# Kernel optimization log

Measured on AMD Instinct MI355X. Metric: run time of the kernel, lower is better.

## Reference

```python
import jax, jax.numpy as jnp
import numpy as np

NEG_SLOPE = 0.2  # PyG GATConv default leaky_relu slope
EPS = 1e-16


def gat_conv(x, W, att_src, att_dst, bias, src, dst, num_nodes, heads, out_ch, concat):
    # x: [N, F_in]; W: [F_in, heads*out_ch]
    h = (x @ W).reshape(num_nodes, heads, out_ch)          # [N, H, C]
    a_src = jnp.sum(h * att_src, axis=-1)                  # [N, H]
    a_dst = jnp.sum(h * att_dst, axis=-1)                  # [N, H]
    alpha = jax.nn.leaky_relu(a_src[src] + a_dst[dst], NEG_SLOPE)  # [E, H]
    # segment softmax over incoming edges of each destination node
    amax = jax.ops.segment_max(alpha, dst, num_segments=num_nodes)  # [N, H]
    ex = jnp.exp(alpha - amax[dst])                        # [E, H]
    denom = jax.ops.segment_sum(ex, dst, num_segments=num_nodes)    # [N, H]
    attn = ex / (denom[dst] + EPS)                         # [E, H]
    msg = h[src] * attn[:, :, None]                        # [E, H, C]
    out = jax.ops.segment_sum(msg, dst, num_segments=num_nodes)     # [N, H, C]
    if concat:
        out = out.reshape(num_nodes, heads * out_ch)
    else:
        out = out.mean(axis=1)
    return out + bias


def setup_inputs() -> dict:
    key = jax.random.key(0)
    ks = jax.random.split(key, 10)
    N, E, F_in, H, C, OUT = 50000, 800000, 512, 4, 64, 40
    x = jax.random.normal(ks[0], (N, F_in), dtype=jnp.float32)
    edge_index = jax.random.randint(ks[1], (2, E), 0, N, dtype=jnp.int64)
    s1 = (2.0 / (F_in + H * C)) ** 0.5
    s2 = (2.0 / (H * C + OUT)) ** 0.5
    return {
        "x": x,
        "edge_index": edge_index,
        "W1": jax.random.normal(ks[2], (F_in, H * C), dtype=jnp.float32) * s1,
        "att_src1": jax.random.normal(ks[3], (H, C), dtype=jnp.float32) * 0.1,
        "att_dst1": jax.random.normal(ks[4], (H, C), dtype=jnp.float32) * 0.1,
        "b1": jnp.zeros((H * C,), dtype=jnp.float32),
        "W2": jax.random.normal(ks[5], (H * C, OUT), dtype=jnp.float32) * s2,
        "att_src2": jax.random.normal(ks[6], (1, OUT), dtype=jnp.float32) * 0.1,
        "att_dst2": jax.random.normal(ks[7], (1, OUT), dtype=jnp.float32) * 0.1,
        "b2": jnp.zeros((OUT,), dtype=jnp.float32),
    }


def reference(x, edge_index, W1, att_src1, att_dst1, b1, W2, att_src2, att_dst2, b2):
    N = x.shape[0]
    H, C = att_src1.shape
    OUT = att_src2.shape[1]
    # PyG GATConv default: add self-loops
    loops = jnp.arange(N, dtype=edge_index.dtype)
    src = jnp.concatenate([edge_index[0], loops])
    dst = jnp.concatenate([edge_index[1], loops])
    # dropout is identity in eval mode
    h = gat_conv(x, W1, att_src1, att_dst1, b1, src, dst, N, H, C, concat=True)
    h = jax.nn.elu(h)
    out = gat_conv(h, W2, att_src2, att_dst2, b2, src, dst, N, 1, OUT, concat=False)
    return jax.nn.log_softmax(out, axis=1)
```

## Files before the change

### kernel.cpp

```cpp
#include <hip/hip_runtime.h>
#include <math.h>

#define FIN   512
#define H1DIM 256
#define HEADS 4
#define CH    64
#define OUTC  40
#define NEG   0.2f
#define EPSV  1e-16f
#define BK    64

__device__ __forceinline__ float leaky(float a) { return fmaxf(a, NEG * a); }

__device__ __forceinline__ short f2bf(float f) {
    unsigned u = __builtin_bit_cast(unsigned, f);
    u += 0x7FFFu + ((u >> 16) & 1u);
    return (short)(u >> 16);
}
__device__ __forceinline__ float bf2f(short s) {
    return __builtin_bit_cast(float, ((unsigned)(unsigned short)s) << 16);
}
__device__ __forceinline__ unsigned cvtpk(float lo, float hi) {
    unsigned r;
    asm("v_cvt_pk_bf16_f32 %0, %1, %2" : "=v"(r) : "v"(lo), "v"(hi));
    return r;
}
__device__ __forceinline__ float lo16(unsigned u) {
    return __builtin_bit_cast(float, u << 16);
}
__device__ __forceinline__ float hi16(unsigned u) {
    return __builtin_bit_cast(float, u & 0xffff0000u);
}

typedef __attribute__((ext_vector_type(8))) short short8;
typedef __attribute__((ext_vector_type(4))) short short4_t;
typedef __attribute__((ext_vector_type(4))) float float4_t;

typedef unsigned int u32;
typedef const __attribute__((address_space(1))) u32 gu32;
typedef __attribute__((address_space(3))) u32 lu32;

__device__ __forceinline__ void load_lds16(const void* g, void* l) {
    __builtin_amdgcn_global_load_lds((gu32*)g, (lu32*)l, 16, 0, 0);
}

__global__ void cvt_w1_kernel(const float* __restrict__ W1, short* __restrict__ w1t)
{
    int idx = blockIdx.x * 256 + threadIdx.x;
    if (idx >= FIN * H1DIM) return;
    int k = idx >> 8;
    int n = idx & 255;
    w1t[(size_t)n * FIN + k] = f2bf(W1[idx]);
}

__global__ __launch_bounds__(256) void gemm1_mfma_kernel(
    const float* __restrict__ x, const short* __restrict__ w1t,
    const float* __restrict__ attS, const float* __restrict__ attD,
    short* __restrict__ h1b, float* __restrict__ aS1, float* __restrict__ aD1, int N)
{
    __shared__ float Alf[64 * BK];
    __shared__ short Bls[256 * BK];

    const int tid  = threadIdx.x;
    const int lane = tid & 63;
    const int wid  = tid >> 6;
    const int row0 = blockIdx.x * 64;
    const int col0 = wid * 64;
    const int quad = lane >> 4;
    const int m16  = lane & 15;

    const int achunk = ((tid & 15) ^ (tid >> 4)) * 4;
    const float* asrcA[4];
#pragma unroll
    for (int p = 0; p < 4; ++p) {
        int r = row0 + p * 16 + (tid >> 4);
        if (r >= N) r = N - 1;
        asrcA[p] = x + (size_t)r * FIN + achunk;
    }

    const int trow = tid >> 3;
    const int bswz = ((tid & 7) ^ (trow & 7)) * 8;
    const short* bsrc[8];
#pragma unroll
    for (int p = 0; p < 8; ++p)
        bsrc[p] = w1t + (size_t)(p * 32 + trow) * FIN + bswz;

    float4_t acc[4][4];
#pragma unroll
    for (int i = 0; i < 4; ++i)
#pragma unroll
        for (int j = 0; j < 4; ++j) acc[i][j] = (float4_t){0.f, 0.f, 0.f, 0.f};

    const int swzB = (m16 & 7);

    for (int k0 = 0; k0 < FIN; k0 += BK) {
#pragma unroll
        for (int p = 0; p < 4; ++p)
            load_lds16(asrcA[p] + k0, Alf + p * 1024 + tid * 4);
#pragma unroll
        for (int p = 0; p < 8; ++p)
            load_lds16(bsrc[p] + k0, Bls + p * 2048 + tid * 8);
        __syncthreads();

#pragma unroll
        for (int half = 0; half < 2; ++half) {
            short8 a[4], b[4];
#pragma unroll
            for (int i = 0; i < 4; ++i) {
                int row = i * 16 + m16;
                int c0 = (quad + 4 * half) * 2;
                float4 f0 = *(const float4*)&Alf[row * BK + ((c0 ^ m16) * 4)];
                float4 f1 = *(const float4*)&Alf[row * BK + (((c0 + 1) ^ m16) * 4)];
                unsigned* tp = (unsigned*)&a[i];
                tp[0] = cvtpk(f0.x, f0.y);
                tp[1] = cvtpk(f0.z, f0.w);
                tp[2] = cvtpk(f1.x, f1.y);
                tp[3] = cvtpk(f1.z, f1.w);
            }
#pragma unroll
            for (int j = 0; j < 4; ++j) {
                int col = col0 + j * 16 + m16;
                int sub = (quad + 4 * half) ^ swzB;
                b[j] = *(const short8*)&Bls[col * BK + sub * 8];
            }
#pragma unroll
            for (int i = 0; i < 4; ++i)
#pragma unroll
                for (int j = 0; j < 4; ++j)
                    acc[i][j] = __builtin_amdgcn_mfma_f32_16x16x32_bf16(a[i], b[j], acc[i][j], 0, 0, 0);
        }
        __syncthreads();
    }

    float attSv[4], attDv[4];
#pragma unroll
    for (int j = 0; j < 4; ++j) {
        attSv[j] = attS[col0 + j * 16 + m16];
        attDv[j] = attD[col0 + j * 16 + m16];
    }

#pragma unroll
    for (int i = 0; i < 4; ++i) {
#pragma unroll
        for (int r = 0; r < 4; ++r) {
            int row = row0 + i * 16 + quad * 4 + r;
            if (row < N) {
#pragma unroll
                for (int j = 0; j < 4; ++j)
                    h1b[(size_t)row * H1DIM + col0 + j * 16 + m16] = f2bf(acc[i][j][r]);
            }
            float ps = acc[i][0][r] * attSv[0] + acc[i][1][r] * attSv[1]
                     + acc[i][2][r] * attSv[2] + acc[i][3][r] * attSv[3];
            float pd = acc[i][0][r] * attDv[0] + acc[i][1][r] * attDv[1]
                     + acc[i][2][r] * attDv[2] + acc[i][3][r] * attDv[3];
#pragma unroll
            for (int off = 1; off < 16; off <<= 1) {
                ps += __shfl_xor(ps, off);
                pd += __shfl_xor(pd, off);
            }
            if (m16 == 0 && row < N) {
                aS1[(size_t)row * 4 + wid] = ps;
                aD1[(size_t)row * 4 + wid] = pd;
            }
        }
    }
}

__global__ void degcount_kernel(const int* __restrict__ ei, int* __restrict__ deg,
                                int E, int Etot)
{
    int e = blockIdx.x * 256 + threadIdx.x;
    if (e >= Etot) return;
    int d = (e < E) ? ei[E + e] : (e - E);
    atomicAdd(&deg[d], 1);
}

__global__ __launch_bounds__(1024) void scan_partial_kernel(
    const int* __restrict__ deg, int* __restrict__ offsets,
    int* __restrict__ bsums, int N)
{
    __shared__ int wsums[16];
    __shared__ int excl[16];
    int tid = threadIdx.x, lane = tid & 63, wid = tid >> 6;
    int idx = blockIdx.x * 1024 + tid;
    int v = (idx < N) ? deg[idx] : 0;
    int sv = v;
#pragma unroll
    for (int off = 1; off < 64; off <<= 1) {
        int t = __shfl_up(sv, off, 64);
        if (lane >= off) sv += t;
    }
    if (lane == 63) wsums[wid] = sv;
    __syncthreads();
    if (wid == 0 && lane < 16) {
        int wv = wsums[lane];
        int sw = wv;
#pragma unroll
        for (int off = 1; off < 16; off <<= 1) {
            int t = __shfl_up(sw, off, 64);
            if (lane >= off) sw += t;
        }
        excl[lane] = sw - wv;
        if (lane == 15) bsums[blockIdx.x] = sw;
    }
    __syncthreads();
    if (idx < N) offsets[idx + 1] = sv + excl[wid];
}

__global__ __launch_bounds__(1024) void scan_tops_kernel(
    int* __restrict__ bsums, int* __restrict__ boffs, int nb)
{
    __shared__ int wsums[16];
    __shared__ int excl[16];
    int tid = threadIdx.x, lane = tid & 63, wid = tid >> 6;
    int v = (tid < nb) ? bsums[tid] : 0;
    int sv = v;
#pragma unroll
    for (int off = 1; off < 64; off <<= 1) {
        int t = __shfl_up(sv, off, 64);
        if (lane >= off) sv += t;
    }
    if (lane == 63) wsums[wid] = sv;
    __syncthreads();
    if (wid == 0 && lane < 16) {
        int wv = wsums[lane];
        int sw = wv;
#pragma unroll
        for (int off = 1; off < 16; off <<= 1) {
            int t = __shfl_up(sw, off, 64);
            if (lane >= off) sw += t;
        }
        excl[lane] = sw - wv;
    }
    __syncthreads();
    if (tid < nb) boffs[tid] = sv + excl[wid] - v;
}

__global__ __launch_bounds__(1024) void scan_add_kernel(
    int* __restrict__ offsets, const int* __restrict__ boffs, int N)
{
    int idx = blockIdx.x * 1024 + threadIdx.x;
    if (idx == 0) offsets[0] = 0;
    if (idx < N) offsets[idx + 1] += boffs[blockIdx.x];
}

__global__ void scatter_kernel(const int* __restrict__ ei, const int* __restrict__ offsets,
                               int* __restrict__ cursor, int* __restrict__ csr_src,
                               int E, int Etot)
{
    int e = blockIdx.x * 256 + threadIdx.x;
    if (e >= Etot) return;
    int s, d;
    if (e < E) { s = ei[e]; d = ei[E + e]; }
    else       { s = e - E; d = s; }
    int pos = offsets[d] + atomicAdd(&cursor[d], 1);
    csr_src[pos] = s;
}

__global__ __launch_bounds__(256) void agg1_kernel(
    const short* __restrict__ h1b, const float* __restrict__ aS,
    const float* __restrict__ aD, const int* __restrict__ offsets,
    const int* __restrict__ csr_src, const float* __restrict__ b1,
    short* __restrict__ g1b, int N)
{
    int lane = threadIdx.x & 63, wid = threadIdx.x >> 6;
    int half = lane >> 5;
    int l32  = lane & 31;
    int n = blockIdx.x * 4 + wid;
    if (n >= N) return;
    int start = offsets[n], end = offsets[n + 1];
    int h = l32 >> 3;
    int cbase = l32 * 8;
    float adh = aD[(size_t)n * 4 + h];

    float ac[8];
#pragma unroll
    for (int c = 0; c < 8; ++c) ac[c] = 0.f;
    float denom = 0.f;

    int p = start;
    for (; p + 4 <= end; p += 4) {
        int sA0 = csr_src[p],     sB0 = csr_src[p + 1];
        int sA1 = csr_src[p + 2], sB1 = csr_src[p + 3];
        int s0 = half ? sB0 : sA0;
        int s1 = half ? sB1 : sA1;
        float t0 = aS[(size_t)s0 * 4 + h] + adh;
        float t1 = aS[(size_t)s1 * 4 + h] + adh;
        short8 r0 = *(const short8*)&h1b[(size_t)s0 * H1DIM + cbase];
        short8 r1 = *(const short8*)&h1b[(size_t)s1 * H1DIM + cbase];
        float w0 = __expf(leaky(t0));
        float w1 = __expf(leaky(t1));
        denom += w0 + w1;
        const unsigned* u0 = (const unsigned*)&r0;
        const unsigned* u1 = (const unsigned*)&r1;
#pragma unroll
        for (int k = 0; k < 4; ++k) {
            ac[2 * k]     += w0 * lo16(u0[k]) + w1 * lo16(u1[k]);
            ac[2 * k + 1] += w0 * hi16(u0[k]) + w1 * hi16(u1[k]);
        }
    }
    for (; p + 2 <= end; p += 2) {
        int sA = csr_src[p], sB = csr_src[p + 1];
        int s = half ? sB : sA;
        float t = aS[(size_t)s * 4 + h] + adh;
        short8 r = *(const short8*)&h1b[(size_t)s * H1DIM + cbase];
        float w = __expf(leaky(t));
        denom += w;
        const unsigned* u = (const unsigned*)&r;
#pragma unroll
        for (int k = 0; k < 4; ++k) {
            ac[2 * k]     += w * lo16(u[k]);
            ac[2 * k + 1] += w * hi16(u[k]);
        }
    }
    if (p < end) {
        int s = csr_src[p];
        float t = aS[(size_t)s * 4 + h] + adh;
        short8 r = *(const short8*)&h1b[(size_t)s * H1DIM + cbase];
        float w = half ? 0.f : __expf(leaky(t));
        denom += w;
        const unsigned* u = (const unsigned*)&r;
#pragma unroll
        for (int k = 0; k < 4; ++k) {
            ac[2 * k]     += w * lo16(u[k]);
            ac[2 * k + 1] += w * hi16(u[k]);
        }
    }

    denom += __shfl_xor(denom, 32);
#pragma unroll
    for (int c = 0; c < 8; ++c) ac[c] += __shfl_xor(ac[c], 32);

    if (half == 0) {
        float inv = 1.f / (denom + EPSV);
        float4 b0 = *(const float4*)&b1[cbase];
        float4 b4 = *(const float4*)&b1[cbase + 4];
        float v[8];
        v[0] = ac[0] * inv + b0.x;
        v[1] = ac[1] * inv + b0.y;
        v[2] = ac[2] * inv + b0.z;
        v[3] = ac[3] * inv + b0.w;
        v[4] = ac[4] * inv + b4.x;
        v[5] = ac[5] * inv + b4.y;
        v[6] = ac[6] * inv + b4.z;
        v[7] = ac[7] * inv + b4.w;
#pragma unroll
        for (int c = 0; c < 8; ++c) v[c] = v[c] > 0.f ? v[c] : expm1f(v[c]);
        short8 o;
        unsigned* op = (unsigned*)&o;
        op[0] = cvtpk(v[0], v[1]);
        op[1] = cvtpk(v[2], v[3]);
        op[2] = cvtpk(v[4], v[5]);
        op[3] = cvtpk(v[6], v[7]);
        *(short8*)&g1b[(size_t)n * H1DIM + cbase] = o;
    }
}

__global__ __launch_bounds__(256) void gemm2_kernel(
    const short* __restrict__ g1b, const float* __restrict__ W2,
    const float* __restrict__ attS2, const float* __restrict__ attD2,
    short* __restrict__ h2b, float* __restrict__ aS2, float* __restrict__ aD2, int N)
{
    __shared__ float rows[4][8][256];
    int lane = threadIdx.x & 63, wid = threadIdx.x >> 6;
    int nbase = blockIdx.x * 32 + wid * 8;
    bool act = lane < OUTC;
    int cc = act ? lane : 0;
    float attS = act ? attS2[lane] : 0.f;
    float attD = act ? attD2[lane] : 0.f;

#pragma unroll
    for (int i = 0; i < 8; ++i) {
        int n = nbase + i;
        float4 v = make_float4(0.f, 0.f, 0.f, 0.f);
        if (n < N) {
            short4_t hv = *(const short4_t*)&g1b[(size_t)n * H1DIM + lane * 4];
            v = make_float4(bf2f(hv[0]), bf2f(hv[1]), bf2f(hv[2]), bf2f(hv[3]));
        }
        *(float4*)&rows[wid][i][lane * 4] = v;
    }

    float acc[8];
#pragma unroll
    for (int i = 0; i < 8; ++i) acc[i] = 0.f;

    for (int k = 0; k < H1DIM; k += 4) {
        float w0 = W2[(size_t)(k + 0) * OUTC + cc];
        float w1 = W2[(size_t)(k + 1) * OUTC + cc];
        float w2 = W2[(size_t)(k + 2) * OUTC + cc];
        float w3 = W2[(size_t)(k + 3) * OUTC + cc];
#pragma unroll
        for (int i = 0; i < 8; ++i) {
            float4 g = *(const float4*)&rows[wid][i][k];
            acc[i] += g.x * w0 + g.y * w1 + g.z * w2 + g.w * w3;
        }
    }

#pragma unroll
    for (int i = 0; i < 8; ++i) {
        int n = nbase + i;
        if (n >= N) continue;
        if (act) h2b[(size_t)n * OUTC + lane] = f2bf(acc[i]);
        float ts = act ? acc[i] * attS : 0.f;
        float td = act ? acc[i] * attD : 0.f;
#pragma unroll
        for (int off = 32; off > 0; off >>= 1) {
            ts += __shfl_xor(ts, off);
            td += __shfl_xor(td, off);
        }
        if (lane == 0) { aS2[n] = ts; aD2[n] = td; }
    }
}

__global__ __launch_bounds__(256) void agg2_kernel(
    const short* __restrict__ h2b, const float* __restrict__ aS2,
    const float* __restrict__ aD2, const int* __restrict__ offsets,
    const int* __restrict__ csr_src, const float* __restrict__ b2,
    float* __restrict__ out, int N)
{
    int lane = threadIdx.x & 63, wid = threadIdx.x >> 6;
    int n = blockIdx.x * 4 + wid;
    if (n >= N) return;
    int start = offsets[n], end = offsets[n + 1];
    bool act = lane < OUTC;
    int cc = act ? lane : 0;
    float ad = aD2[n];

    float acc = 0.f, denom = 0.f;
    int p = start;
    for (; p + 4 <= end; p += 4) {
        int s0 = csr_src[p], s1 = csr_src[p + 1], s2 = csr_src[p + 2], s3 = csr_src[p + 3];
        float w0 = __expf(leaky(aS2[s0] + ad));
        float w1 = __expf(leaky(aS2[s1] + ad));
        float w2 = __expf(leaky(aS2[s2] + ad));
        float w3 = __expf(leaky(aS2[s3] + ad));
        short v0 = h2b[(size_t)s0 * OUTC + cc];
        short v1 = h2b[(size_t)s1 * OUTC + cc];
        short v2 = h2b[(size_t)s2 * OUTC + cc];
        short v3 = h2b[(size_t)s3 * OUTC + cc];
        denom += w0 + w1 + w2 + w3;
        acc += w0 * bf2f(v0) + w1 * bf2f(v1) + w2 * bf2f(v2) + w3 * bf2f(v3);
    }
    for (; p < end; ++p) {
        int s = csr_src[p];
        float w = __expf(leaky(aS2[s] + ad));
        denom += w;
        acc += w * bf2f(h2b[(size_t)s * OUTC + cc]);
    }

    float v = acc / (denom + EPSV) + (act ? b2[lane] : 0.f);

    float vm = act ? v : -INFINITY;
#pragma unroll
    for (int off = 32; off > 0; off >>= 1) vm = fmaxf(vm, __shfl_xor(vm, off));
    float ex2 = act ? __expf(v - vm) : 0.f;
    float tot = ex2;
#pragma unroll
    for (int off = 32; off > 0; off >>= 1) tot += __shfl_xor(tot, off);
    float res = v - vm - __logf(tot);
    if (act) out[(size_t)n * OUTC + lane] = res;
}

extern "C" void kernel_launch(void* const* d_in, const int* in_sizes, int n_in,
                              void* d_out, int out_size, void* d_ws, size_t ws_size,
                              hipStream_t stream)
{
    const float* x     = (const float*)d_in[0];
    const int*   ei    = (const int*)d_in[1];
    const float* W1    = (const float*)d_in[2];
    const float* attS1 = (const float*)d_in[3];
    const float* attD1 = (const float*)d_in[4];
    const float* b1    = (const float*)d_in[5];
    const float* W2    = (const float*)d_in[6];
    const float* attS2 = (const float*)d_in[7];
    const float* attD2 = (const float*)d_in[8];
    const float* b2    = (const float*)d_in[9];
    float* out = (float*)d_out;

    const int N    = in_sizes[0] / FIN;
    const int E    = in_sizes[1] / 2;
    const int Etot = E + N;
    const int nb   = (N + 1023) / 1024;

    char* ws = (char*)d_ws;
    size_t off = 0;
    auto take = [&](size_t bytes) -> char* {
        char* p = ws + off;
        off = (off + bytes + 255) & ~(size_t)255;
        return p;
    };
    short* h1b     = (short*)take((size_t)N * H1DIM * 2);
    short* g1b     = (short*)take((size_t)N * H1DIM * 2);
    short* w1t     = (short*)take((size_t)FIN * H1DIM * 2);
    float* aS1     = (float*)take((size_t)N * 4 * 4);
    float* aD1     = (float*)take((size_t)N * 4 * 4);
    short* h2b     = (short*)take((size_t)N * OUTC * 2);
    float* aS2v    = (float*)take((size_t)N * 4);
    float* aD2v    = (float*)take((size_t)N * 4);
    int*   degcur  = (int*)take((size_t)2 * N * 4);
    int*   deg     = degcur;
    int*   cursor  = degcur + N;
    int*   offsets = (int*)take((size_t)(N + 1) * 4);
    int*   bsums   = (int*)take((size_t)nb * 4);
    int*   boffs   = (int*)take((size_t)nb * 4);
    int*   csr_src = (int*)take((size_t)Etot * 4);

    hipMemsetAsync(degcur, 0, (size_t)2 * N * 4, stream);

    cvt_w1_kernel<<<(FIN * H1DIM + 255) / 256, 256, 0, stream>>>(W1, w1t);
    gemm1_mfma_kernel<<<(N + 63) / 64, 256, 0, stream>>>(x, w1t, attS1, attD1, h1b, aS1, aD1, N);
    degcount_kernel<<<(Etot + 255) / 256, 256, 0, stream>>>(ei, deg, E, Etot);
    scan_partial_kernel<<<nb, 1024, 0, stream>>>(deg, offsets, bsums, N);
    scan_tops_kernel<<<1, 1024, 0, stream>>>(bsums, boffs, nb);
    scan_add_kernel<<<nb, 1024, 0, stream>>>(offsets, boffs, N);
    scatter_kernel<<<(Etot + 255) / 256, 256, 0, stream>>>(ei, offsets, cursor, csr_src, E, Etot);
    agg1_kernel<<<(N + 3) / 4, 256, 0, stream>>>(h1b, aS1, aD1, offsets, csr_src, b1, g1b, N);
    gemm2_kernel<<<(N + 31) / 32, 256, 0, stream>>>(g1b, W2, attS2, attD2, h2b, aS2v, aD2v, N);
    agg2_kernel<<<(N + 3) / 4, 256, 0, stream>>>(h2b, aS2v, aD2v, offsets, csr_src, b2, out, N);
}
```

Baseline: 433.2 us.

## Record edge ranks during degree count and batch-load CSR indices with shuffles

The degree-count kernel now saves each edge's atomic return value as its rank, so the scatter kernel writes its CSR position directly without a second round of atomics on a cursor array. The aggregation kernels load up to 64 neighbor indices per wave with one coalesced read and broadcast them with __shfl, replacing repeated scalar csr_src loads inside the edge loops. Tail edges are masked by zero weight, which adds some padded iterations. The rank array costs an extra Etot-sized buffer write and read.

Result: no change. 436.6 us (+0.8%).

```diff
diff --git a/kernel.cpp b/kernel.cpp
--- a/kernel.cpp
+++ b/kernel.cpp
@@ -167,12 +167,12 @@
 }
 
 __global__ void degcount_kernel(const int* __restrict__ ei, int* __restrict__ deg,
-                                int E, int Etot)
+                                int* __restrict__ rank, int E, int Etot)
 {
     int e = blockIdx.x * 256 + threadIdx.x;
     if (e >= Etot) return;
     int d = (e < E) ? ei[E + e] : (e - E);
-    atomicAdd(&deg[d], 1);
+    rank[e] = atomicAdd(&deg[d], 1);
 }
 
 __global__ __launch_bounds__(1024) void scan_partial_kernel(
@@ -245,7 +245,7 @@
 }
 
 __global__ void scatter_kernel(const int* __restrict__ ei, const int* __restrict__ offsets,
-                               int* __restrict__ cursor, int* __restrict__ csr_src,
+                               const int* __restrict__ rank, int* __restrict__ csr_src,
                                int E, int Etot)
 {
     int e = blockIdx.x * 256 + threadIdx.x;
@@ -253,8 +253,7 @@
     int s, d;
     if (e < E) { s = ei[e]; d = ei[E + e]; }
     else       { s = e - E; d = s; }
-    int pos = offsets[d] + atomicAdd(&cursor[d], 1);
-    csr_src[pos] = s;
+    csr_src[offsets[d] + rank[e]] = s;
 }
 
 __global__ __launch_bounds__(256) void agg1_kernel(
@@ -269,6 +268,7 @@
     int n = blockIdx.x * 4 + wid;
     if (n >= N) return;
     int start = offsets[n], end = offsets[n + 1];
+    int deg = end - start;
     int h = l32 >> 3;
     int cbase = l32 * 8;
     float adh = aD[(size_t)n * 4 + h];
@@ -278,52 +278,25 @@
     for (int c = 0; c < 8; ++c) ac[c] = 0.f;
     float denom = 0.f;
 
-    int p = start;
-    for (; p + 4 <= end; p += 4) {
-        int sA0 = csr_src[p],     sB0 = csr_src[p + 1];
-        int sA1 = csr_src[p + 2], sB1 = csr_src[p + 3];
-        int s0 = half ? sB0 : sA0;
-        int s1 = half ? sB1 : sA1;
-        float t0 = aS[(size_t)s0 * 4 + h] + adh;
-        float t1 = aS[(size_t)s1 * 4 + h] + adh;
-        short8 r0 = *(const short8*)&h1b[(size_t)s0 * H1DIM + cbase];
-        short8 r1 = *(const short8*)&h1b[(size_t)s1 * H1DIM + cbase];
-        float w0 = __expf(leaky(t0));
-        float w1 = __expf(leaky(t1));
-        denom += w0 + w1;
-        const unsigned* u0 = (const unsigned*)&r0;
-        const unsigned* u1 = (const unsigned*)&r1;
-#pragma unroll
-        for (int k = 0; k < 4; ++k) {
-            ac[2 * k]     += w0 * lo16(u0[k]) + w1 * lo16(u1[k]);
-            ac[2 * k + 1] += w0 * hi16(u0[k]) + w1 * hi16(u1[k]);
-        }
-    }
-    for (; p + 2 <= end; p += 2) {
-        int sA = csr_src[p], sB = csr_src[p + 1];
-        int s = half ? sB : sA;
-        float t = aS[(size_t)s * 4 + h] + adh;
-        short8 r = *(const short8*)&h1b[(size_t)s * H1DIM + cbase];
-        float w = __expf(leaky(t));
-        denom += w;
-        const unsigned* u = (const unsigned*)&r;
-#pragma unroll
-        for (int k = 0; k < 4; ++k) {
-            ac[2 * k]     += w * lo16(u[k]);
-            ac[2 * k + 1] += w * hi16(u[k]);
-        }
-    }
-    if (p < end) {
-        int s = csr_src[p];
-        float t = aS[(size_t)s * 4 + h] + adh;
-        short8 r = *(const short8*)&h1b[(size_t)s * H1DIM + cbase];
-        float w = half ? 0.f : __expf(leaky(t));
-        denom += w;
-        const unsigned* u = (const unsigned*)&r;
-#pragma unroll
-        for (int k = 0; k < 4; ++k) {
-            ac[2 * k]     += w * lo16(u[k]);
-            ac[2 * k + 1] += w * hi16(u[k]);
+    for (int c0 = 0; c0 < deg; c0 += 64) {
+        int cnt = deg - c0; if (cnt > 64) cnt = 64;
+        int idx = csr_src[start + c0 + (lane < cnt ? lane : cnt - 1)];
+        for (int e0 = 0; e0 < cnt; e0 += 8) {
+#pragma unroll
+            for (int q = 0; q < 4; ++q) {
+                int e = e0 + 2 * q + half;
+                int s = __shfl(idx, e);
+                float t = aS[(size_t)s * 4 + h] + adh;
+                float w = (e < cnt) ? __expf(leaky(t)) : 0.f;
+                short8 r = *(const short8*)&h1b[(size_t)s * H1DIM + cbase];
+                denom += w;
+                const unsigned* u = (const unsigned*)&r;
+#pragma unroll
+                for (int k = 0; k < 4; ++k) {
+                    ac[2 * k]     += w * lo16(u[k]);
+                    ac[2 * k + 1] += w * hi16(u[k]);
+                }
+            }
         }
     }
 
@@ -422,30 +395,27 @@
     int n = blockIdx.x * 4 + wid;
     if (n >= N) return;
     int start = offsets[n], end = offsets[n + 1];
+    int deg = end - start;
     bool act = lane < OUTC;
     int cc = act ? lane : 0;
     float ad = aD2[n];
 
     float acc = 0.f, denom = 0.f;
-    int p = start;
-    for (; p + 4 <= end; p += 4) {
-        int s0 = csr_src[p], s1 = csr_src[p + 1], s2 = csr_src[p + 2], s3 = csr_src[p + 3];
-        float w0 = __expf(leaky(aS2[s0] + ad));
-        float w1 = __expf(leaky(aS2[s1] + ad));
-        float w2 = __expf(leaky(aS2[s2] + ad));
-        float w3 = __expf(leaky(aS2[s3] + ad));
-        short v0 = h2b[(size_t)s0 * OUTC + cc];
-        short v1 = h2b[(size_t)s1 * OUTC + cc];
-        short v2 = h2b[(size_t)s2 * OUTC + cc];
-        short v3 = h2b[(size_t)s3 * OUTC + cc];
-        denom += w0 + w1 + w2 + w3;
-        acc += w0 * bf2f(v0) + w1 * bf2f(v1) + w2 * bf2f(v2) + w3 * bf2f(v3);
-    }
-    for (; p < end; ++p) {
-        int s = csr_src[p];
-        float w = __expf(leaky(aS2[s] + ad));
-        denom += w;
-        acc += w * bf2f(h2b[(size_t)s * OUTC + cc]);
+    for (int c0 = 0; c0 < deg; c0 += 64) {
+        int cnt = deg - c0; if (cnt > 64) cnt = 64;
+        int idx = csr_src[start + c0 + (lane < cnt ? lane : cnt - 1)];
+        for (int e0 = 0; e0 < cnt; e0 += 4) {
+#pragma unroll
+            for (int q = 0; q < 4; ++q) {
+                int e = e0 + q;
+                int s = __shfl(idx, e);
+                float t = aS2[s] + ad;
+                float w = (e < cnt) ? __expf(leaky(t)) : 0.f;
+                short hv = h2b[(size_t)s * OUTC + cc];
+                denom += w;
+                acc += w * bf2f(hv);
+            }
+        }
     }
 
     float v = acc / (denom + EPSV) + (act ? b2[lane] : 0.f);
@@ -497,23 +467,22 @@
     short* h2b     = (short*)take((size_t)N * OUTC * 2);
     float* aS2v    = (float*)take((size_t)N * 4);
     float* aD2v    = (float*)take((size_t)N * 4);
-    int*   degcur  = (int*)take((size_t)2 * N * 4);
-    int*   deg     = degcur;
-    int*   cursor  = degcur + N;
+    int*   deg     = (int*)take((size_t)N * 4);
     int*   offsets = (int*)take((size_t)(N + 1) * 4);
     int*   bsums   = (int*)take((size_t)nb * 4);
     int*   boffs   = (int*)take((size_t)nb * 4);
+    int*   rank    = (int*)take((size_t)Etot * 4);
     int*   csr_src = (int*)take((size_t)Etot * 4);
 
-    hipMemsetAsync(degcur, 0, (size_t)2 * N * 4, stream);
+    hipMemsetAsync(deg, 0, (size_t)N * 4, stream);
 
     cvt_w1_kernel<<<(FIN * H1DIM + 255) / 256, 256, 0, stream>>>(W1, w1t);
     gemm1_mfma_kernel<<<(N + 63) / 64, 256, 0, stream>>>(x, w1t, attS1, attD1, h1b, aS1, aD1, N);
-    degcount_kernel<<<(Etot + 255) / 256, 256, 0, stream>>>(ei, deg, E, Etot);
+    degcount_kernel<<<(Etot + 255) / 256, 256, 0, stream>>>(ei, deg, rank, E, Etot);
     scan_partial_kernel<<<nb, 1024, 0, stream>>>(deg, offsets, bsums, N);
     scan_tops_kernel<<<1, 1024, 0, stream>>>(bsums, boffs, nb);
     scan_add_kernel<<<nb, 1024, 0, stream>>>(offsets, boffs, N);
-    scatter_kernel<<<(Etot + 255) / 256, 256, 0, stream>>>(ei, offsets, cursor, csr_src, E, Etot);
+    scatter_kernel<<<(Etot + 255) / 256, 256, 0, stream>>>(ei, offsets, rank, csr_src, E, Etot);
     agg1_kernel<<<(N + 3) / 4, 256, 0, stream>>>(h1b, aS1, aD1, offsets, csr_src, b1, g1b, N);
     gemm2_kernel<<<(N + 31) / 32, 256, 0, stream>>>(g1b, W2, attS2, attD2, h2b, aS2v, aD2v, N);
     agg2_kernel<<<(N + 3) / 4, 256, 0, stream>>>(h2b, aS2v, aD2v, offsets, csr_src, b2, out, N);
```

## Store layer-1 features as FP8 and reuse degree-count atomic rank for CSR scatter

Applied to the files above, without the earlier changes.

Layer-1 projected features h1 are now written as FP8 (e4m3 via packed convert) instead of bf16, halving the bytes gathered per edge in the aggregation kernel. The degree-count kernel records each edge's atomic return value as its rank, so the scatter kernel no longer needs a second atomic pass over a cursor array. The FP8 storage reduces gather bandwidth at the cost of considerably lower precision in the attention-weighted sums. The rank array adds one extra Etot-sized buffer write and read. GEMM output stores become byte-granular scattered writes.

After: 389.4 us. -10.1%, faster.

```diff
diff --git a/kernel.cpp b/kernel.cpp
--- a/kernel.cpp
+++ b/kernel.cpp
@@ -32,6 +32,16 @@
     return __builtin_bit_cast(float, u & 0xffff0000u);
 }
 
+typedef __attribute__((ext_vector_type(2))) float floatx2;
+
+__device__ __forceinline__ unsigned f32x2_to_fp8x2(float a, float b) {
+    return (unsigned)__builtin_amdgcn_cvt_pk_fp8_f32(a, b, 0, false);
+}
+template <bool HI>
+__device__ __forceinline__ floatx2 fp8x2_to_f32(unsigned u) {
+    return __builtin_amdgcn_cvt_pk_f32_fp8((int)u, HI);
+}
+
 typedef __attribute__((ext_vector_type(8))) short short8;
 typedef __attribute__((ext_vector_type(4))) short short4_t;
 typedef __attribute__((ext_vector_type(4))) float float4_t;
@@ -56,7 +66,7 @@
 __global__ __launch_bounds__(256) void gemm1_mfma_kernel(
     const float* __restrict__ x, const short* __restrict__ w1t,
     const float* __restrict__ attS, const float* __restrict__ attD,
-    short* __restrict__ h1b, float* __restrict__ aS1, float* __restrict__ aD1, int N)
+    unsigned char* __restrict__ h1f, float* __restrict__ aS1, float* __restrict__ aD1, int N)
 {
     __shared__ float Alf[64 * BK];
     __shared__ short Bls[256 * BK];
@@ -145,9 +155,13 @@
         for (int r = 0; r < 4; ++r) {
             int row = row0 + i * 16 + quad * 4 + r;
             if (row < N) {
-#pragma unroll
-                for (int j = 0; j < 4; ++j)
-                    h1b[(size_t)row * H1DIM + col0 + j * 16 + m16] = f2bf(acc[i][j][r]);
+                unsigned pa = f32x2_to_fp8x2(acc[i][0][r], acc[i][1][r]);
+                unsigned pb = f32x2_to_fp8x2(acc[i][2][r], acc[i][3][r]);
+                unsigned char* hp = h1f + (size_t)row * H1DIM + col0 + m16;
+                hp[0]  = (unsigned char)(pa & 0xff);
+                hp[16] = (unsigned char)((pa >> 8) & 0xff);
+                hp[32] = (unsigned char)(pb & 0xff);
+                hp[48] = (unsigned char)((pb >> 8) & 0xff);
             }
             float ps = acc[i][0][r] * attSv[0] + acc[i][1][r] * attSv[1]
                      + acc[i][2][r] * attSv[2] + acc[i][3][r] * attSv[3];
@@ -167,12 +181,12 @@
 }
 
 __global__ void degcount_kernel(const int* __restrict__ ei, int* __restrict__ deg,
-                                int E, int Etot)
+                                int* __restrict__ rank, int E, int Etot)
 {
     int e = blockIdx.x * 256 + threadIdx.x;
     if (e >= Etot) return;
     int d = (e < E) ? ei[E + e] : (e - E);
-    atomicAdd(&deg[d], 1);
+    rank[e] = atomicAdd(&deg[d], 1);
 }
 
 __global__ __launch_bounds__(1024) void scan_partial_kernel(
@@ -245,7 +259,7 @@
 }
 
 __global__ void scatter_kernel(const int* __restrict__ ei, const int* __restrict__ offsets,
-                               int* __restrict__ cursor, int* __restrict__ csr_src,
+                               const int* __restrict__ rank, int* __restrict__ csr_src,
                                int E, int Etot)
 {
     int e = blockIdx.x * 256 + threadIdx.x;
@@ -253,12 +267,11 @@
     int s, d;
     if (e < E) { s = ei[e]; d = ei[E + e]; }
     else       { s = e - E; d = s; }
-    int pos = offsets[d] + atomicAdd(&cursor[d], 1);
-    csr_src[pos] = s;
+    csr_src[offsets[d] + rank[e]] = s;
 }
 
 __global__ __launch_bounds__(256) void agg1_kernel(
-    const short* __restrict__ h1b, const float* __restrict__ aS,
+    const unsigned char* __restrict__ h1f, const float* __restrict__ aS,
     const float* __restrict__ aD, const int* __restrict__ offsets,
     const int* __restrict__ csr_src, const float* __restrict__ b1,
     short* __restrict__ g1b, int N)
@@ -286,45 +299,50 @@
         int s1 = half ? sB1 : sA1;
         float t0 = aS[(size_t)s0 * 4 + h] + adh;
         float t1 = aS[(size_t)s1 * 4 + h] + adh;
-        short8 r0 = *(const short8*)&h1b[(size_t)s0 * H1DIM + cbase];
-        short8 r1 = *(const short8*)&h1b[(size_t)s1 * H1DIM + cbase];
+        uint2 r0 = *(const uint2*)&h1f[(size_t)s0 * H1DIM + cbase];
+        uint2 r1 = *(const uint2*)&h1f[(size_t)s1 * H1DIM + cbase];
         float w0 = __expf(leaky(t0));
         float w1 = __expf(leaky(t1));
         denom += w0 + w1;
-        const unsigned* u0 = (const unsigned*)&r0;
-        const unsigned* u1 = (const unsigned*)&r1;
-#pragma unroll
-        for (int k = 0; k < 4; ++k) {
-            ac[2 * k]     += w0 * lo16(u0[k]) + w1 * lo16(u1[k]);
-            ac[2 * k + 1] += w0 * hi16(u0[k]) + w1 * hi16(u1[k]);
-        }
+        floatx2 d0a = fp8x2_to_f32<false>(r0.x), d0b = fp8x2_to_f32<true>(r0.x);
+        floatx2 d0c = fp8x2_to_f32<false>(r0.y), d0d = fp8x2_to_f32<true>(r0.y);
+        floatx2 d1a = fp8x2_to_f32<false>(r1.x), d1b = fp8x2_to_f32<true>(r1.x);
+        floatx2 d1c = fp8x2_to_f32<false>(r1.y), d1d = fp8x2_to_f32<true>(r1.y);
+        ac[0] += w0 * d0a.x + w1 * d1a.x;
+        ac[1] += w0 * d0a.y + w1 * d1a.y;
+        ac[2] += w0 * d0b.x + w1 * d1b.x;
+        ac[3] += w0 * d0b.y + w1 * d1b.y;
+        ac[4] += w0 * d0c.x + w1 * d1c.x;
+        ac[5] += w0 * d0c.y + w1 * d1c.y;
+        ac[6] += w0 * d0d.x + w1 * d1d.x;
+        ac[7] += w0 * d0d.y + w1 * d1d.y;
     }
     for (; p + 2 <= end; p += 2) {
         int sA = csr_src[p], sB = csr_src[p + 1];
         int s = half ? sB : sA;
         float t = aS[(size_t)s * 4 + h] + adh;
-        short8 r = *(const short8*)&h1b[(size_t)s * H1DIM + cbase];
+        uint2 r = *(const uint2*)&h1f[(size_t)s * H1DIM + cbase];
         float w = __expf(leaky(t));
         denom += w;
-        const unsigned* u = (const unsigned*)&r;
-#pragma unroll
-        for (int k = 0; k < 4; ++k) {
-            ac[2 * k]     += w * lo16(u[k]);
-            ac[2 * k + 1] += w * hi16(u[k]);
-        }
+        floatx2 da = fp8x2_to_f32<false>(r.x), db = fp8x2_to_f32<true>(r.x);
+        floatx2 dc = fp8x2_to_f32<false>(r.y), dd = fp8x2_to_f32<true>(r.y);
+        ac[0] += w * da.x; ac[1] += w * da.y;
+        ac[2] += w * db.x; ac[3] += w * db.y;
+        ac[4] += w * dc.x; ac[5] += w * dc.y;
+        ac[6] += w * dd.x; ac[7] += w * dd.y;
     }
     if (p < end) {
         int s = csr_src[p];
         float t = aS[(size_t)s * 4 + h] + adh;
-        short8 r = *(const short8*)&h1b[(size_t)s * H1DIM + cbase];
+        uint2 r = *(const uint2*)&h1f[(size_t)s * H1DIM + cbase];
         float w = half ? 0.f : __expf(leaky(t));
         denom += w;
-        const unsigned* u = (const unsigned*)&r;
-#pragma unroll
-        for (int k = 0; k < 4; ++k) {
-            ac[2 * k]     += w * lo16(u[k]);
-            ac[2 * k + 1] += w * hi16(u[k]);
-        }
+        floatx2 da = fp8x2_to_f32<false>(r.x), db = fp8x2_to_f32<true>(r.x);
+        floatx2 dc = fp8x2_to_f32<false>(r.y), dd = fp8x2_to_f32<true>(r.y);
+        ac[0] += w * da.x; ac[1] += w * da.y;
+        ac[2] += w * db.x; ac[3] += w * db.y;
+        ac[4] += w * dc.x; ac[5] += w * dc.y;
+        ac[6] += w * dd.x; ac[7] += w * dd.y;
     }
 
     denom += __shfl_xor(denom, 32);
@@ -489,7 +507,7 @@
         off = (off + bytes + 255) & ~(size_t)255;
         return p;
     };
-    short* h1b     = (short*)take((size_t)N * H1DIM * 2);
+    unsigned char* h1f = (unsigned char*)take((size_t)N * H1DIM);
     short* g1b     = (short*)take((size_t)N * H1DIM * 2);
     short* w1t     = (short*)take((size_t)FIN * H1DIM * 2);
     float* aS1     = (float*)take((size_t)N * 4 * 4);
@@ -497,24 +515,23 @@
     short* h2b     = (short*)take((size_t)N * OUTC * 2);
     float* aS2v    = (float*)take((size_t)N * 4);
     float* aD2v    = (float*)take((size_t)N * 4);
-    int*   degcur  = (int*)take((size_t)2 * N * 4);
-    int*   deg     = degcur;
-    int*   cursor  = degcur + N;
+    int*   deg     = (int*)take((size_t)N * 4);
     int*   offsets = (int*)take((size_t)(N + 1) * 4);
     int*   bsums   = (int*)take((size_t)nb * 4);
     int*   boffs   = (int*)take((size_t)nb * 4);
+    int*   rank    = (int*)take((size_t)Etot * 4);
     int*   csr_src = (int*)take((size_t)Etot * 4);
 
-    hipMemsetAsync(degcur, 0, (size_t)2 * N * 4, stream);
+    (void)hipMemsetAsync(deg, 0, (size_t)N * 4, stream);
 
     cvt_w1_kernel<<<(FIN * H1DIM + 255) / 256, 256, 0, stream>>>(W1, w1t);
-    gemm1_mfma_kernel<<<(N + 63) / 64, 256, 0, stream>>>(x, w1t, attS1, attD1, h1b, aS1, aD1, N);
-    degcount_kernel<<<(Etot + 255) / 256, 256, 0, stream>>>(ei, deg, E, Etot);
+    gemm1_mfma_kernel<<<(N + 63) / 64, 256, 0, stream>>>(x, w1t, attS1, attD1, h1f, aS1, aD1, N);
+    degcount_kernel<<<(Etot + 255) / 256, 256, 0, stream>>>(ei, deg, rank, E, Etot);
     scan_partial_kernel<<<nb, 1024, 0, stream>>>(deg, offsets, bsums, N);
     scan_tops_kernel<<<1, 1024, 0, stream>>>(bsums, boffs, nb);
     scan_add_kernel<<<nb, 1024, 0, stream>>>(offsets, boffs, N);
-    scatter_kernel<<<(Etot + 255) / 256, 256, 0, stream>>>(ei, offsets, cursor, csr_src, E, Etot);
-    agg1_kernel<<<(N + 3) / 4, 256, 0, stream>>>(h1b, aS1, aD1, offsets, csr_src, b1, g1b, N);
+    scatter_kernel<<<(Etot + 255) / 256, 256, 0, stream>>>(ei, offsets, rank, csr_src, E, Etot);
+    agg1_kernel<<<(N + 3) / 4, 256, 0, stream>>>(h1f, aS1, aD1, offsets, csr_src, b1, g1b, N);
     gemm2_kernel<<<(N + 31) / 32, 256, 0, stream>>>(g1b, W2, attS2, attD2, h2b, aS2v, aD2v, N);
     agg2_kernel<<<(N + 3) / 4, 256, 0, stream>>>(h2b, aS2v, aD2v, offsets, csr_src, b2, out, N);
 }
```
